# Optimization experiments

Measured on AMD Instinct MI355X. Metric: run time of the kernel, lower is better.

## Reference

```python
import jax, jax.numpy as jnp
import numpy as np

B, H, W, C = 1, 64, 64, 768
NUM_HEADS = 12
HEAD_DIM = C // NUM_HEADS  # 64


def setup_inputs() -> dict:
    key = jax.random.key(0)
    ks = jax.random.split(key, 7)
    s = 0.02
    return {
        "imagelike_bhwc": jax.random.normal(ks[0], (B, H, W, C), dtype=jnp.float32),
        "qkv_w": jax.random.normal(ks[1], (C, 3 * C), dtype=jnp.float32) * s,
        "qkv_b": jax.random.normal(ks[2], (3 * C,), dtype=jnp.float32) * s,
        "proj_w": jax.random.normal(ks[3], (C, C), dtype=jnp.float32) * s,
        "proj_b": jax.random.normal(ks[4], (C,), dtype=jnp.float32) * s,
        "rel_pos_h": jax.random.normal(ks[5], (2 * H - 1, HEAD_DIM), dtype=jnp.float32) * s,
        "rel_pos_w": jax.random.normal(ks[6], (2 * W - 1, HEAD_DIM), dtype=jnp.float32) * s,
    }


def reference(imagelike_bhwc, qkv_w, qkv_b, proj_w, proj_b, rel_pos_h, rel_pos_w):
    b, h, w, c = imagelike_bhwc.shape
    n = h * w
    nh, hd = NUM_HEADS, c // NUM_HEADS
    scale = hd ** (-0.5)

    # qkv projection -> (3, B*nh, N, hd)
    qkv = imagelike_bhwc @ qkv_w + qkv_b  # (b,h,w,3c)
    qkv = qkv.reshape(b, n, 3, nh, hd).transpose(2, 0, 3, 1, 4).reshape(3, b * nh, n, hd)
    q, k, v = qkv[0], qkv[1], qkv[2]

    # scaled dot-product scores
    attn = jnp.einsum("bqd,bkd->bqk", q * scale, k)  # (b*nh, n, n)

    # decomposed relative position bias (query grid == key grid == base grid)
    idx_h = jnp.arange(h)[:, None] - jnp.arange(h)[None, :] + (h - 1)  # (h,h)
    idx_w = jnp.arange(w)[:, None] - jnp.arange(w)[None, :] + (w - 1)  # (w,w)
    Rh = rel_pos_h[idx_h]  # (h, h, hd)
    Rw = rel_pos_w[idx_w]  # (w, w, hd)
    r_q = q.reshape(b * nh, h, w, hd)
    rel_h = jnp.einsum("bhwc,hkc->bhwk", r_q, Rh)  # (b*nh, h, w, h)
    rel_w = jnp.einsum("bhwc,wkc->bhwk", r_q, Rw)  # (b*nh, h, w, w)
    bias = (rel_h[:, :, :, :, None] + rel_w[:, :, :, None, :]).reshape(b * nh, n, n)

    attn = jax.nn.softmax(attn + bias, axis=-1)
    out = jnp.einsum("bqk,bkd->bqd", attn, v)  # (b*nh, n, hd)

    out = out.reshape(b, nh, h, w, hd).transpose(0, 2, 3, 1, 4).reshape(b, h, w, c)
    return out @ proj_w + proj_b
```

## Files before the change

### kernel.cpp

```cpp
#include <hip/hip_runtime.h>
#include <stdint.h>

typedef unsigned short u16;
typedef __bf16 bf16x8 __attribute__((ext_vector_type(8)));
typedef float f32x4 __attribute__((ext_vector_type(4)));
typedef unsigned short ushort8 __attribute__((ext_vector_type(8)));
typedef unsigned short ushort4v __attribute__((ext_vector_type(4)));

#define MFMA __builtin_amdgcn_mfma_f32_16x16x32_bf16
#define EXP2 __builtin_amdgcn_exp2f

__device__ __forceinline__ u16 f2bf(float f){
  uint32_t u = __builtin_bit_cast(uint32_t, f);
  u += 0x7fffu + ((u >> 16) & 1u);
  return (u16)(u >> 16);
}
__device__ __forceinline__ float bf2f(u16 h){
  uint32_t u = ((uint32_t)h) << 16;
  return __builtin_bit_cast(float, u);
}
__device__ __forceinline__ uint32_t cvtpk(float lo, float hi){
  uint32_t r;
  asm("v_cvt_pk_bf16_f32 %0, %1, %2" : "=v"(r) : "v"(lo), "v"(hi));
  return r;
}
__device__ __forceinline__ bf16x8 ld8(const u16* p){
  return __builtin_bit_cast(bf16x8, *(const ushort8*)p);
}
__device__ __forceinline__ void gload16(const void* g, void* l){
  __builtin_amdgcn_global_load_lds((__attribute__((address_space(1))) void*)(void*)g,
                                   (__attribute__((address_space(3))) void*)l, 16, 0, 0);
}


__device__ __forceinline__ void tr_body(const float* __restrict__ in, u16* __restrict__ out,
                                        int R, int Cc, int bx, int by, int t, float* tile ){
  int r0 = bx*64, c0 = by*64;
  int c = t & 63, r4 = t >> 6;
  for (int i = 0; i < 16; ++i)
    tile[(r4 + i*4)*65 + c] = in[(size_t)(r0 + r4 + i*4)*Cc + c0 + c];
  __syncthreads();
  for (int i = 0; i < 16; ++i){
    int rr = r4 + i*4;
    out[(size_t)(c0 + rr)*R + r0 + c] = f2bf(tile[c*65 + rr]);
  }
}

__global__ __launch_bounds__(256) void k_prep(const float* __restrict__ X32,
                                              const float* __restrict__ qkvw,
                                              const float* __restrict__ projw,
                                              const float* __restrict__ rposh,
                                              const float* __restrict__ rposw,
                                              u16* __restrict__ Xb, u16* __restrict__ W1T,
                                              u16* __restrict__ PT,
                                              u16* __restrict__ rh8, u16* __restrict__ rw8){
  __shared__ float tile[64*65];
  const int b = blockIdx.x, t = threadIdx.x;
  if (b < 1536){
    int i = b*256 + t;
    const float4* p = (const float4*)X32;
    float4 a = p[i*2], c = p[i*2+1];
    ushort8 o;
    o[0]=f2bf(a.x); o[1]=f2bf(a.y); o[2]=f2bf(a.z); o[3]=f2bf(a.w);
    o[4]=f2bf(c.x); o[5]=f2bf(c.y); o[6]=f2bf(c.z); o[7]=f2bf(c.w);
    ((ushort8*)Xb)[i] = o;
  } else if (b < 1968){
    int bb = b - 1536;
    tr_body(qkvw, W1T, 768, 2304, bb % 12, bb / 12, t, tile);
  } else if (b < 2112){
    int bb = b - 1968;
    tr_body(projw, PT, 768, 768, bb % 12, bb / 12, t, tile);
  } else {
    int i = (b - 2112)*256 + t;
    if (i < 8192)      rh8[i] = f2bf(i < 8128 ? rposh[i]*8.0f : 0.0f);
    else { int j = i - 8192; rw8[j] = f2bf(j < 8128 ? rposw[j]*8.0f : 0.0f); }
  }
}


__global__ __launch_bounds__(256) void k_qkv(const u16* __restrict__ X, const u16* __restrict__ WT,
                                             const float* __restrict__ bias,
                                             u16* __restrict__ Qs, u16* __restrict__ Kf, u16* __restrict__ Vf){
  __shared__ __align__(16) u16 At[128*64];
  __shared__ __align__(16) u16 Bt[128*64];
  __shared__ __align__(16) u16 Tt[4][64*72];
  const int tid = threadIdx.x, lane = tid & 63, w = tid >> 6;
  const int m0 = blockIdx.x*128, n0 = blockIdx.y*128;
  const int wr = (w >> 1)*64, wc = (w & 1)*64;
  const int lr = lane & 15, lg = lane >> 4;
  const int srcRow = w*32 + (lane >> 3);
  const int srcK   = (lane & 7)*8;
  f32x4 acc[4][4] = {};
  for (int kt = 0; kt < 12; ++kt){
    const int kbase = kt*64;
    for (int s = 0; s < 4; ++s){
      gload16(X  + (size_t)(m0 + srcRow + s*8)*768 + kbase + srcK, At + (w*32 + s*8)*64);
      gload16(WT + (size_t)(n0 + srcRow + s*8)*768 + kbase + srcK, Bt + (w*32 + s*8)*64);
    }
    __syncthreads();
    bf16x8 af[2][4], bfr[2][4];
    for (int ks = 0; ks < 2; ++ks)
      for (int i = 0; i < 4; ++i){
        af[ks][i]  = ld8(At + (wr + i*16 + lr)*64 + ks*32 + lg*8);
        bfr[ks][i] = ld8(Bt + (wc + i*16 + lr)*64 + ks*32 + lg*8);
      }
    for (int ks = 0; ks < 2; ++ks)
      for (int mi = 0; mi < 4; ++mi)
        for (int ni = 0; ni < 4; ++ni)
          acc[mi][ni] = MFMA(af[ks][mi], bfr[ks][ni], acc[mi][ni], 0, 0, 0);
    __syncthreads();
  }
  const int colbase = n0 + wc;
  const int s3 = colbase / 768;
  const int hh = (colbase % 768) >> 6;
  const int rowbase = m0 + wr;
  if (s3 == 0){
    for (int mi = 0; mi < 4; ++mi)
      for (int ni = 0; ni < 4; ++ni){
        float bv = bias[colbase + ni*16 + lr];
        for (int r = 0; r < 4; ++r){
          int row = rowbase + mi*16 + lg*4 + r;
          Qs[((size_t)hh*4096 + row)*64 + ni*16 + lr] =
              f2bf((acc[mi][ni][r] + bv)*(0.125f*1.44269504f));
        }
      }
  } else {
    u16* T = Tt[w];
    for (int mi = 0; mi < 4; ++mi)
      for (int ni = 0; ni < 4; ++ni){
        float bv = bias[colbase + ni*16 + lr];
        for (int r = 0; r < 4; ++r){
          int row_l = mi*16 + lg*4 + r, col_l = ni*16 + lr;
          u16 v = f2bf(acc[mi][ni][r] + bv);
          if (s3 == 1) T[row_l*72 + col_l] = v;
          else         T[col_l*72 + row_l] = v;
        }
      }
    const int kb = rowbase >> 6;
    u16* dst = (s3 == 1 ? Kf : Vf) + ((size_t)hh*64 + kb)*4096 + lane*8;
    #pragma unroll
    for (int f = 0; f < 8; ++f){
      int a = f >> 1, ks = f & 1;
      *(ushort8*)&dst[f*512] = *(const ushort8*)&T[(a*16 + lr)*72 + ks*32 + lg*8];
    }
  }
}


__global__ __launch_bounds__(256) void k_rel(const u16* __restrict__ Qs, const u16* __restrict__ Rh8,
                                             const u16* __restrict__ Rw8,
                                             u16* __restrict__ relh, u16* __restrict__ relw){
  __shared__ __align__(16) u16 Ql[64*64];
  __shared__ __align__(16) u16 Rhl[64*64];
  __shared__ __align__(16) u16 Rwl[128*64];
  const int tid = threadIdx.x, lane = tid & 63, w = tid >> 6;
  const int qh = blockIdx.x, h = blockIdx.y;
  const int lr = lane & 15, lg = lane >> 4;
  for (int j = 0; j < 2; ++j){
    int ch = tid + 256*j;
    int row = ch >> 3, k8 = (ch & 7)*8;
    *(ushort8*)&Ql[row*64 + k8]  = *(const ushort8*)&Qs[((size_t)h*4096 + qh*64 + row)*64 + k8];
    *(ushort8*)&Rhl[row*64 + k8] = *(const ushort8*)&Rh8[(qh + row)*64 + k8];
  }
  for (int j = 0; j < 4; ++j){
    int ch = tid + 256*j;
    int row = ch >> 3, k8 = (ch & 7)*8;
    *(ushort8*)&Rwl[row*64 + k8] = *(const ushort8*)&Rw8[row*64 + k8];
  }
  __syncthreads();
  bf16x8 a[2];
  for (int ks = 0; ks < 2; ++ks) a[ks] = ld8(Ql + (w*16 + lr)*64 + ks*32 + lg*8);
  for (int ct = 0; ct < 4; ++ct){
    f32x4 c = {};
    for (int ks = 0; ks < 2; ++ks)
      c = MFMA(a[ks], ld8(Rhl + (ct*16 + lr)*64 + ks*32 + lg*8), c, 0, 0, 0);
    int kh = 63 - (ct*16 + lr);
    for (int r = 0; r < 4; ++r){
      int qw = w*16 + lg*4 + r;
      relh[((size_t)h*4096 + qh*64 + qw)*64 + kh] = f2bf(c[r]);
    }
  }
  for (int ct = 0; ct < 8; ++ct){
    f32x4 c = {};
    for (int ks = 0; ks < 2; ++ks)
      c = MFMA(a[ks], ld8(Rwl + (ct*16 + lr)*64 + ks*32 + lg*8), c, 0, 0, 0);
    int cc = ct*16 + lr;
    for (int r = 0; r < 4; ++r){
      int qw = w*16 + lg*4 + r;
      int kw = qw + 63 - cc;
      if (kw >= 0 && kw < 64)
        relw[((size_t)h*4096 + qh*64 + qw)*64 + kw] = f2bf(c[r]);
    }
  }
}


__global__ __launch_bounds__(256, 3) void k_flash(const u16* __restrict__ Qs, const u16* __restrict__ Kf,
                                                  const u16* __restrict__ Vf,
                                                  const u16* __restrict__ relh, const u16* __restrict__ relw,
                                                  u16* __restrict__ Ob){
  __shared__ __align__(16) u16 Vl[2][4096];
  __shared__ __align__(16) char Psm[4][2048];
  const int tid = threadIdx.x, lane = tid & 63, w = tid >> 6;
  const int b = blockIdx.x;
  const int p = (b & 7)*96 + (b >> 3);
  const int h = p >> 6, qb = p & 63;
  const int lr = lane & 15, lg = lane >> 4;
  const size_t hq = (size_t)h*4096;
  const int q = qb*64 + w*16 + lr;
  char* Pb = Psm[w];
  const int swz = (lr & 7) << 4;

  const bf16x8 qf0 = ld8(Qs + (hq + q)*64 + lg*8);
  const bf16x8 qf1 = ld8(Qs + (hq + q)*64 + 32 + lg*8);
  float rwf[4][4];
  #pragma unroll
  for (int ct = 0; ct < 4; ++ct){
    ushort4v t = *(const ushort4v*)&relw[(hq + q)*64 + ct*16 + lg*4];
    #pragma unroll
    for (int r = 0; r < 4; ++r) rwf[ct][r] = bf2f(t[r]);
  }

  const u16* KfH = Kf + (size_t)h*262144 + lane*8;
  const u16* VfH = Vf + (size_t)h*262144;
  const u16* rhbase = relh + (hq + q)*64;

  float m = -1e30f, lsum = 0.f;
  f32x4 oacc[4] = {};
  bf16x8 kA[8], kB[8];

  auto loadK = [&](bf16x8 (&dst)[8], int kbi){
    const u16* kp = KfH + kbi*4096;
    #pragma unroll
    for (int f = 0; f < 8; ++f) dst[f] = ld8(kp + f*512);
  };
  auto stageV = [&](int buf, int kb){
    const u16* vs = VfH + kb*4096 + w*1024 + lane*8;
    gload16(vs,       &Vl[buf][w*1024]);
    gload16(vs + 512, &Vl[buf][w*1024 + 512]);
  };

#define ITERBODY(KB, KC, BUF)                                                 \
  {                                                                           \
    const u16* VL = Vl[BUF] + lane*8;                                         \
    const float rhv = bf2f(rhbase[KB]);                                       \
    f32x4 s[4];                                                               \
    _Pragma("unroll")                                                         \
    for (int ct = 0; ct < 4; ++ct){                                           \
      _Pragma("unroll")                                                       \
      for (int r = 0; r < 4; ++r) s[ct][r] = rhv + rwf[ct][r];                \
    }                                                                         \
    __builtin_amdgcn_s_setprio(1);                                            \
    _Pragma("unroll")                                                         \
    for (int ct = 0; ct < 4; ++ct){                                           \
      s[ct] = MFMA(KC[ct*2],   qf0, s[ct], 0, 0, 0);                          \
      s[ct] = MFMA(KC[ct*2+1], qf1, s[ct], 0, 0, 0);                          \
    }                                                                         \
    __builtin_amdgcn_s_setprio(0);                                            \
                                       \
    float pm0 = fmaxf(fmaxf(s[0][0], s[0][1]), fmaxf(fmaxf(s[0][2], s[0][3]), \
                      fmaxf(s[1][0], s[1][1])));                              \
    float pm1 = fmaxf(fmaxf(s[1][2], s[1][3]), fmaxf(fmaxf(s[2][0], s[2][1]), \
                      fmaxf(s[2][2], s[2][3])));                              \
    float pm2 = fmaxf(fmaxf(s[3][0], s[3][1]), fmaxf(s[3][2], s[3][3]));      \
    float pm = fmaxf(fmaxf(pm0, pm1), pm2);                                   \
             \
    if (__any(pm > m)){                                                       \
      pm = fmaxf(pm, __shfl_xor(pm, 16, 64));                                 \
      pm = fmaxf(pm, __shfl_xor(pm, 32, 64));                                 \
      const float nm = fmaxf(m, pm);                                          \
      const float corr = EXP2(m - nm);                                        \
      m = nm;                                                                 \
      lsum *= corr;                                                           \
      _Pragma("unroll")                                                       \
      for (int dt = 0; dt < 4; ++dt)                                          \
        _Pragma("unroll")                                                     \
        for (int r = 0; r < 4; ++r) oacc[dt][r] *= corr;                      \
    }                                                                         \
    float rs = 0.f;                                                           \
    _Pragma("unroll")                                                         \
    for (int ct = 0; ct < 4; ++ct){                                           \
      _Pragma("unroll")                                                       \
      for (int r = 0; r < 4; ++r){                                            \
        float p2 = EXP2(s[ct][r] - m);                                        \
        s[ct][r] = p2; rs += p2;                                              \
      }                                                                       \
    }                                                                         \
    lsum += rs;                           \
    _Pragma("unroll")                                                         \
    for (int ct = 0; ct < 4; ++ct){                                           \
      uint2 uv;                                                               \
      uv.x = cvtpk(s[ct][0], s[ct][1]);                                       \
      uv.y = cvtpk(s[ct][2], s[ct][3]);                                       \
      *(uint2*)(Pb + ((lr*128 + ct*32 + lg*8) ^ swz)) = uv;                   \
    }                                                                         \
    bf16x8 pa0 = __builtin_bit_cast(bf16x8, *(ushort8*)(Pb + ((lr*128      + lg*16) ^ swz))); \
    bf16x8 pa1 = __builtin_bit_cast(bf16x8, *(ushort8*)(Pb + ((lr*128 + 64 + lg*16) ^ swz))); \
    __builtin_amdgcn_s_setprio(1);                                            \
    _Pragma("unroll")                                                         \
    for (int dt = 0; dt < 4; ++dt){                                           \
      oacc[dt] = MFMA(ld8(VL + (dt*2)*512),   pa0, oacc[dt], 0, 0, 0);        \
      oacc[dt] = MFMA(ld8(VL + (dt*2+1)*512), pa1, oacc[dt], 0, 0, 0);        \
    }                                                                         \
    __builtin_amdgcn_s_setprio(0);                                            \
  }

  loadK(kA, 0);
  stageV(0, 0);
  __syncthreads();
  for (int kb2 = 0; kb2 < 64; kb2 += 2){
    stageV(1, (kb2 + 1) & 63);
    loadK(kB, (kb2 + 1) & 63);
    ITERBODY(kb2, kA, 0)
    __syncthreads();
    stageV(0, (kb2 + 2) & 63);
    loadK(kA, (kb2 + 2) & 63);
    ITERBODY(kb2 + 1, kB, 1)
    __syncthreads();
  }
#undef ITERBODY

  lsum += __shfl_xor(lsum, 16, 64);
  lsum += __shfl_xor(lsum, 32, 64);
  const float inv = 1.0f / lsum;
  #pragma unroll
  for (int dt = 0; dt < 4; ++dt){
    ushort4v pk;
    #pragma unroll
    for (int r = 0; r < 4; ++r) pk[r] = f2bf(oacc[dt][r]*inv);
    *(ushort4v*)&Ob[(size_t)q*768 + h*64 + dt*16 + lg*4] = pk;
  }
}


__global__ __launch_bounds__(256) void k_proj(const u16* __restrict__ A, const u16* __restrict__ WT,
                                              const float* __restrict__ bias, float* __restrict__ out){
  __shared__ __align__(16) u16 At[128*64];
  __shared__ __align__(16) u16 Bt[128*64];
  const int tid = threadIdx.x, lane = tid & 63, w = tid >> 6;
  const int m0 = blockIdx.x*128, n0 = blockIdx.y*128;
  const int wr = (w >> 1)*64, wc = (w & 1)*64;
  const int lr = lane & 15, lg = lane >> 4;
  const int srcRow = w*32 + (lane >> 3);
  const int srcK   = (lane & 7)*8;
  f32x4 acc[4][4] = {};
  for (int kt = 0; kt < 12; ++kt){
    const int kbase = kt*64;
    for (int s = 0; s < 4; ++s){
      gload16(A  + (size_t)(m0 + srcRow + s*8)*768 + kbase + srcK, At + (w*32 + s*8)*64);
      gload16(WT + (size_t)(n0 + srcRow + s*8)*768 + kbase + srcK, Bt + (w*32 + s*8)*64);
    }
    __syncthreads();
    bf16x8 af[2][4], bfr[2][4];
    for (int ks = 0; ks < 2; ++ks)
      for (int i = 0; i < 4; ++i){
        af[ks][i]  = ld8(At + (wr + i*16 + lr)*64 + ks*32 + lg*8);
        bfr[ks][i] = ld8(Bt + (wc + i*16 + lr)*64 + ks*32 + lg*8);
      }
    for (int ks = 0; ks < 2; ++ks)
      for (int mi = 0; mi < 4; ++mi)
        for (int ni = 0; ni < 4; ++ni)
          acc[mi][ni] = MFMA(af[ks][mi], bfr[ks][ni], acc[mi][ni], 0, 0, 0);
    __syncthreads();
  }
  for (int mi = 0; mi < 4; ++mi)
    for (int ni = 0; ni < 4; ++ni){
      int col = n0 + wc + ni*16 + lr;
      float bv = bias[col];
      for (int r = 0; r < 4; ++r){
        int row = m0 + wr + mi*16 + lg*4 + r;
        out[(size_t)row*768 + col] = acc[mi][ni][r] + bv;
      }
    }
}


extern "C" void kernel_launch(void* const* d_in, const int* in_sizes, int n_in,
                              void* d_out, int out_size, void* d_ws, size_t ws_size,
                              hipStream_t stream){
  const float* X32   = (const float*)d_in[0];
  const float* qkvw  = (const float*)d_in[1];
  const float* qkvb  = (const float*)d_in[2];
  const float* projw = (const float*)d_in[3];
  const float* projb = (const float*)d_in[4];
  const float* rposh = (const float*)d_in[5];
  const float* rposw = (const float*)d_in[6];

  u16* Xb  = (u16*)d_ws;
  u16* W1T = Xb  + 3145728;
  u16* PT  = W1T + 1769472;
  u16* Rh8 = PT  + 589824;
  u16* Rw8 = Rh8 + 8192;
  u16* Qs  = Rw8 + 8192;
  u16* Kf  = Qs  + 3145728;
  u16* Vf  = Kf  + 3145728;
  u16* Rlh = Vf  + 3145728;
  u16* Rlw = Rlh + 3145728;
  u16* Ob  = Rlw + 3145728;
  float* out = (float*)d_out;

  k_prep <<<2176, 256, 0, stream>>>(X32, qkvw, projw, rposh, rposw, Xb, W1T, PT, Rh8, Rw8);
  k_qkv  <<<dim3(32, 18), 256, 0, stream>>>(Xb, W1T, qkvb, Qs, Kf, Vf);
  k_rel  <<<dim3(64, 12), 256, 0, stream>>>(Qs, Rh8, Rw8, Rlh, Rlw);
  k_flash<<<768, 256, 0, stream>>>(Qs, Kf, Vf, Rlh, Rlw, Ob);
  k_proj <<<dim3(32, 6), 256, 0, stream>>>(Ob, PT, projb, out);
}
```

Measured before the change: 179.6 us.

## Split flash attention key range across two wave groups with LDS merge

```diff
diff --git a/kernel.cpp b/kernel.cpp
--- a/kernel.cpp
+++ b/kernel.cpp
@@ -195,21 +195,24 @@
 }
 
 
-__global__ __launch_bounds__(256, 3) void k_flash(const u16* __restrict__ Qs, const u16* __restrict__ Kf,
+__global__ __launch_bounds__(512, 4) void k_flash(const u16* __restrict__ Qs, const u16* __restrict__ Kf,
                                                   const u16* __restrict__ Vf,
                                                   const u16* __restrict__ relh, const u16* __restrict__ relw,
                                                   u16* __restrict__ Ob){
-  __shared__ __align__(16) u16 Vl[2][4096];
-  __shared__ __align__(16) char Psm[4][2048];
+  __shared__ __align__(16) char SMEM[81920];
+  u16*  KlB = (u16*)SMEM;
+  u16*  VlB = (u16*)(SMEM + 32768);
   const int tid = threadIdx.x, lane = tid & 63, w = tid >> 6;
   const int b = blockIdx.x;
   const int p = (b & 7)*96 + (b >> 3);
   const int h = p >> 6, qb = p & 63;
+  const int half = w >> 2, qt = w & 3;
   const int lr = lane & 15, lg = lane >> 4;
   const size_t hq = (size_t)h*4096;
-  const int q = qb*64 + w*16 + lr;
-  char* Pb = Psm[w];
+  const int q = qb*64 + qt*16 + lr;
+  char* Pb = SMEM + 65536 + w*2048;
   const int swz = (lr & 7) << 4;
+  const int kb0 = half*32;
 
   const bf16x8 qf0 = ld8(Qs + (hq + q)*64 + lg*8);
   const bf16x8 qf1 = ld8(Qs + (hq + q)*64 + 32 + lg*8);
@@ -221,28 +224,30 @@
     for (int r = 0; r < 4; ++r) rwf[ct][r] = bf2f(t[r]);
   }
 
-  const u16* KfH = Kf + (size_t)h*262144 + lane*8;
+  const u16* KfH = Kf + (size_t)h*262144;
   const u16* VfH = Vf + (size_t)h*262144;
   const u16* rhbase = relh + (hq + q)*64;
 
   float m = -1e30f, lsum = 0.f;
   f32x4 oacc[4] = {};
-  bf16x8 kA[8], kB[8];
-
-  auto loadK = [&](bf16x8 (&dst)[8], int kbi){
-    const u16* kp = KfH + kbi*4096;
-    #pragma unroll
-    for (int f = 0; f < 8; ++f) dst[f] = ld8(kp + f*512);
+
+  auto stage = [&](int buf, int kl){
+    const int tile = half*32 + kl;
+    const int i4 = (w & 3)*1024;
+    const u16* ks = KfH + tile*4096 + i4 + lane*8;
+    const u16* vs = VfH + tile*4096 + i4 + lane*8;
+    u16* kd = KlB + (half*2 + buf)*4096 + i4;
+    u16* vd = VlB + (half*2 + buf)*4096 + i4;
+    gload16(ks,       kd);
+    gload16(ks + 512, kd + 512);
+    gload16(vs,       vd);
+    gload16(vs + 512, vd + 512);
   };
-  auto stageV = [&](int buf, int kb){
-    const u16* vs = VfH + kb*4096 + w*1024 + lane*8;
-    gload16(vs,       &Vl[buf][w*1024]);
-    gload16(vs + 512, &Vl[buf][w*1024 + 512]);
-  };
-
-#define ITERBODY(KB, KC, BUF)                                                 \
+
+#define ITERBODY(KB, BUF)                                                     \
   {                                                                           \
-    const u16* VL = Vl[BUF] + lane*8;                                         \
+    const u16* KL = KlB + (half*2 + (BUF))*4096 + lane*8;                     \
+    const u16* VL = VlB + (half*2 + (BUF))*4096 + lane*8;                     \
     const float rhv = bf2f(rhbase[KB]);                                       \
     f32x4 s[4];                                                               \
     _Pragma("unroll")                                                         \
@@ -253,8 +258,8 @@
     __builtin_amdgcn_s_setprio(1);                                            \
     _Pragma("unroll")                                                         \
     for (int ct = 0; ct < 4; ++ct){                                           \
-      s[ct] = MFMA(KC[ct*2],   qf0, s[ct], 0, 0, 0);                          \
-      s[ct] = MFMA(KC[ct*2+1], qf1, s[ct], 0, 0, 0);                          \
+      s[ct] = MFMA(ld8(KL + (ct*2)*512),   qf0, s[ct], 0, 0, 0);              \
+      s[ct] = MFMA(ld8(KL + (ct*2+1)*512), qf1, s[ct], 0, 0, 0);              \
     }                                                                         \
     __builtin_amdgcn_s_setprio(0);                                            \
                                        \
@@ -286,7 +291,7 @@
         s[ct][r] = p2; rs += p2;                                              \
       }                                                                       \
     }                                                                         \
-    lsum += rs;                           \
+    lsum += rs;                                                               \
     _Pragma("unroll")                                                         \
     for (int ct = 0; ct < 4; ++ct){                                           \
       uint2 uv;                                                               \
@@ -305,30 +310,57 @@
     __builtin_amdgcn_s_setprio(0);                                            \
   }
 
-  loadK(kA, 0);
-  stageV(0, 0);
+  stage(0, 0);
   __syncthreads();
-  for (int kb2 = 0; kb2 < 64; kb2 += 2){
-    stageV(1, (kb2 + 1) & 63);
-    loadK(kB, (kb2 + 1) & 63);
-    ITERBODY(kb2, kA, 0)
-    __syncthreads();
-    stageV(0, (kb2 + 2) & 63);
-    loadK(kA, (kb2 + 2) & 63);
-    ITERBODY(kb2 + 1, kB, 1)
+  for (int kl = 0; kl < 32; kl += 2){
+    stage(1, kl + 1);
+    ITERBODY(kb0 + kl, 0)
+    __syncthreads();
+    if (kl < 30) stage(0, kl + 2);
+    ITERBODY(kb0 + kl + 1, 1)
     __syncthreads();
   }
 #undef ITERBODY
 
   lsum += __shfl_xor(lsum, 16, 64);
   lsum += __shfl_xor(lsum, 32, 64);
-  const float inv = 1.0f / lsum;
-  #pragma unroll
-  for (int dt = 0; dt < 4; ++dt){
-    ushort4v pk;
+  {
+    float* Ow = (float*)SMEM + w*1088;
     #pragma unroll
-    for (int r = 0; r < 4; ++r) pk[r] = f2bf(oacc[dt][r]*inv);
-    *(ushort4v*)&Ob[(size_t)q*768 + h*64 + dt*16 + lg*4] = pk;
+    for (int dt = 0; dt < 4; ++dt)
+      *(f32x4*)&Ow[lr*68 + dt*16 + lg*4] = oacc[dt];
+    if (lg == 0){
+      float* ML = (float*)(SMEM + 34816) + w*32;
+      ML[lr] = m;
+      ML[16 + lr] = lsum;
+    }
+  }
+  __syncthreads();
+  {
+    const int qt2 = tid >> 7, q16 = (tid >> 3) & 15, dq = tid & 7;
+    const int w0 = qt2, w1 = qt2 + 4;
+    const float* ML0 = (const float*)(SMEM + 34816) + w0*32;
+    const float* ML1 = (const float*)(SMEM + 34816) + w1*32;
+    const float m0 = ML0[q16], m1 = ML1[q16];
+    const float l0 = ML0[16 + q16], l1 = ML1[16 + q16];
+    const float ms = fmaxf(m0, m1);
+    const float s0 = EXP2(m0 - ms), s1 = EXP2(m1 - ms);
+    const float inv = 1.0f / (s0*l0 + s1*l1);
+    const float* O0 = (const float*)SMEM + w0*1088 + q16*68 + dq*8;
+    const float* O1 = (const float*)SMEM + w1*1088 + q16*68 + dq*8;
+    f32x4 a0 = *(const f32x4*)O0, a1 = *(const f32x4*)(O0 + 4);
+    f32x4 b0 = *(const f32x4*)O1, b1 = *(const f32x4*)(O1 + 4);
+    float v[8];
+    #pragma unroll
+    for (int j = 0; j < 4; ++j){
+      v[j]     = (s0*a0[j] + s1*b0[j])*inv;
+      v[j + 4] = (s0*a1[j] + s1*b1[j])*inv;
+    }
+    uint4 outv;
+    outv.x = cvtpk(v[0], v[1]); outv.y = cvtpk(v[2], v[3]);
+    outv.z = cvtpk(v[4], v[5]); outv.w = cvtpk(v[6], v[7]);
+    const int qg = qb*64 + qt2*16 + q16;
+    *(uint4*)&Ob[(size_t)qg*768 + h*64 + dq*8] = outv;
   }
 }
 
@@ -402,6 +434,6 @@
   k_prep <<<2176, 256, 0, stream>>>(X32, qkvw, projw, rposh, rposw, Xb, W1T, PT, Rh8, Rw8);
   k_qkv  <<<dim3(32, 18), 256, 0, stream>>>(Xb, W1T, qkvb, Qs, Kf, Vf);
   k_rel  <<<dim3(64, 12), 256, 0, stream>>>(Qs, Rh8, Rw8, Rlh, Rlw);
-  k_flash<<<768, 256, 0, stream>>>(Qs, Kf, Vf, Rlh, Rlw, Ob);
+  k_flash<<<768, 512, 0, stream>>>(Qs, Kf, Vf, Rlh, Rlw, Ob);
   k_proj <<<dim3(32, 6), 256, 0, stream>>>(Ob, PT, projb, out);
 }
```

New measurement: 176.3 us. No clear change (-1.8%).

## Stage K through shared memory and feed P to PV MFMA from registers

Applied to the files above, without the earlier changes.

```diff
diff --git a/kernel.cpp b/kernel.cpp
--- a/kernel.cpp
+++ b/kernel.cpp
@@ -6,6 +6,7 @@
 typedef float f32x4 __attribute__((ext_vector_type(4)));
 typedef unsigned short ushort8 __attribute__((ext_vector_type(8)));
 typedef unsigned short ushort4v __attribute__((ext_vector_type(4)));
+typedef uint32_t uint4v __attribute__((ext_vector_type(4)));
 
 #define MFMA __builtin_amdgcn_mfma_f32_16x16x32_bf16
 #define EXP2 __builtin_amdgcn_exp2f
@@ -138,10 +139,24 @@
       }
     const int kb = rowbase >> 6;
     u16* dst = (s3 == 1 ? Kf : Vf) + ((size_t)hh*64 + kb)*4096 + lane*8;
-    #pragma unroll
-    for (int f = 0; f < 8; ++f){
-      int a = f >> 1, ks = f & 1;
-      *(ushort8*)&dst[f*512] = *(const ushort8*)&T[(a*16 + lr)*72 + ks*32 + lg*8];
+    if (s3 == 1){
+      #pragma unroll
+      for (int f = 0; f < 8; ++f){
+        int a = f >> 1, ks = f & 1;
+        *(ushort8*)&dst[f*512] = *(const ushort8*)&T[(a*16 + lr)*72 + ks*32 + lg*8];
+      }
+    } else {
+      #pragma unroll
+      for (int f = 0; f < 8; ++f){
+        int a = f >> 1, ks = f & 1;
+        const int rowb = (a*16 + lr)*72 + ks*32 + lg*4;
+        ushort4v lo = *(const ushort4v*)&T[rowb];
+        ushort4v hi = *(const ushort4v*)&T[rowb + 16];
+        ushort8 o;
+        o[0]=lo[0]; o[1]=lo[1]; o[2]=lo[2]; o[3]=lo[3];
+        o[4]=hi[0]; o[5]=hi[1]; o[6]=hi[2]; o[7]=hi[3];
+        *(ushort8*)&dst[f*512] = o;
+      }
     }
   }
 }
@@ -199,8 +214,8 @@
                                                   const u16* __restrict__ Vf,
                                                   const u16* __restrict__ relh, const u16* __restrict__ relw,
                                                   u16* __restrict__ Ob){
+  __shared__ __align__(16) u16 Kl[2][4096];
   __shared__ __align__(16) u16 Vl[2][4096];
-  __shared__ __align__(16) char Psm[4][2048];
   const int tid = threadIdx.x, lane = tid & 63, w = tid >> 6;
   const int b = blockIdx.x;
   const int p = (b & 7)*96 + (b >> 3);
@@ -208,8 +223,6 @@
   const int lr = lane & 15, lg = lane >> 4;
   const size_t hq = (size_t)h*4096;
   const int q = qb*64 + w*16 + lr;
-  char* Pb = Psm[w];
-  const int swz = (lr & 7) << 4;
 
   const bf16x8 qf0 = ld8(Qs + (hq + q)*64 + lg*8);
   const bf16x8 qf1 = ld8(Qs + (hq + q)*64 + 32 + lg*8);
@@ -221,27 +234,25 @@
     for (int r = 0; r < 4; ++r) rwf[ct][r] = bf2f(t[r]);
   }
 
-  const u16* KfH = Kf + (size_t)h*262144 + lane*8;
+  const u16* KfH = Kf + (size_t)h*262144;
   const u16* VfH = Vf + (size_t)h*262144;
   const u16* rhbase = relh + (hq + q)*64;
 
   float m = -1e30f, lsum = 0.f;
   f32x4 oacc[4] = {};
-  bf16x8 kA[8], kB[8];
-
-  auto loadK = [&](bf16x8 (&dst)[8], int kbi){
-    const u16* kp = KfH + kbi*4096;
-    #pragma unroll
-    for (int f = 0; f < 8; ++f) dst[f] = ld8(kp + f*512);
-  };
-  auto stageV = [&](int buf, int kb){
+
+  auto stage = [&](int buf, int kb){
+    const u16* ks = KfH + kb*4096 + w*1024 + lane*8;
     const u16* vs = VfH + kb*4096 + w*1024 + lane*8;
+    gload16(ks,       &Kl[buf][w*1024]);
+    gload16(ks + 512, &Kl[buf][w*1024 + 512]);
     gload16(vs,       &Vl[buf][w*1024]);
     gload16(vs + 512, &Vl[buf][w*1024 + 512]);
   };
 
-#define ITERBODY(KB, KC, BUF)                                                 \
+#define ITERBODY(KB, BUF)                                                     \
   {                                                                           \
+    const u16* KL = Kl[BUF] + lane*8;                                         \
     const u16* VL = Vl[BUF] + lane*8;                                         \
     const float rhv = bf2f(rhbase[KB]);                                       \
     f32x4 s[4];                                                               \
@@ -253,8 +264,8 @@
     __builtin_amdgcn_s_setprio(1);                                            \
     _Pragma("unroll")                                                         \
     for (int ct = 0; ct < 4; ++ct){                                           \
-      s[ct] = MFMA(KC[ct*2],   qf0, s[ct], 0, 0, 0);                          \
-      s[ct] = MFMA(KC[ct*2+1], qf1, s[ct], 0, 0, 0);                          \
+      s[ct] = MFMA(ld8(KL + (ct*2)*512),   qf0, s[ct], 0, 0, 0);              \
+      s[ct] = MFMA(ld8(KL + (ct*2+1)*512), qf1, s[ct], 0, 0, 0);              \
     }                                                                         \
     __builtin_amdgcn_s_setprio(0);                                            \
                                        \
@@ -287,15 +298,14 @@
       }                                                                       \
     }                                                                         \
     lsum += rs;                           \
-    _Pragma("unroll")                                                         \
-    for (int ct = 0; ct < 4; ++ct){                                           \
-      uint2 uv;                                                               \
-      uv.x = cvtpk(s[ct][0], s[ct][1]);                                       \
-      uv.y = cvtpk(s[ct][2], s[ct][3]);                                       \
-      *(uint2*)(Pb + ((lr*128 + ct*32 + lg*8) ^ swz)) = uv;                   \
-    }                                                                         \
-    bf16x8 pa0 = __builtin_bit_cast(bf16x8, *(ushort8*)(Pb + ((lr*128      + lg*16) ^ swz))); \
-    bf16x8 pa1 = __builtin_bit_cast(bf16x8, *(ushort8*)(Pb + ((lr*128 + 64 + lg*16) ^ swz))); \
+             \
+    uint4v u0, u1;                                                            \
+    u0[0] = cvtpk(s[0][0], s[0][1]); u0[1] = cvtpk(s[0][2], s[0][3]);         \
+    u0[2] = cvtpk(s[1][0], s[1][1]); u0[3] = cvtpk(s[1][2], s[1][3]);         \
+    u1[0] = cvtpk(s[2][0], s[2][1]); u1[1] = cvtpk(s[2][2], s[2][3]);         \
+    u1[2] = cvtpk(s[3][0], s[3][1]); u1[3] = cvtpk(s[3][2], s[3][3]);         \
+    bf16x8 pa0 = __builtin_bit_cast(bf16x8, u0);                              \
+    bf16x8 pa1 = __builtin_bit_cast(bf16x8, u1);                              \
     __builtin_amdgcn_s_setprio(1);                                            \
     _Pragma("unroll")                                                         \
     for (int dt = 0; dt < 4; ++dt){                                           \
@@ -305,17 +315,14 @@
     __builtin_amdgcn_s_setprio(0);                                            \
   }
 
-  loadK(kA, 0);
-  stageV(0, 0);
+  stage(0, 0);
   __syncthreads();
   for (int kb2 = 0; kb2 < 64; kb2 += 2){
-    stageV(1, (kb2 + 1) & 63);
-    loadK(kB, (kb2 + 1) & 63);
-    ITERBODY(kb2, kA, 0)
-    __syncthreads();
-    stageV(0, (kb2 + 2) & 63);
-    loadK(kA, (kb2 + 2) & 63);
-    ITERBODY(kb2 + 1, kB, 1)
+    stage(1, (kb2 + 1) & 63);
+    ITERBODY(kb2, 0)
+    __syncthreads();
+    stage(0, (kb2 + 2) & 63);
+    ITERBODY(kb2 + 1, 1)
     __syncthreads();
   }
 #undef ITERBODY
```

After: 162.0 us. -9.8%, faster.
